# Optimization experiments

Measured on AMD Instinct MI355X. Metric: run time of the kernel, lower is better.

The kernel has to match this reference:

```python
import jax, jax.numpy as jnp
import numpy as np

JITTER = 1e-06  # from init kwarg
NUM_EMBEDDING = 64

def setup_inputs() -> dict:
    key = jax.random.key(0)
    B, T = 8, 2048
    num_features = 1 + NUM_EMBEDDING + 1 + 1  # mean + z + v + hetero-noise
    tensor = jax.random.normal(key, (B, T, num_features), dtype=jnp.float32)
    return {"tensor": tensor}

def reference(tensor):
    # tensor: (B, T, F) with F = 1 + D + 1 + 1 (mean, z, v, noise)
    B, T, _ = tensor.shape
    mean = tensor[:, :, 0]                       # (B, T)
    z = tensor[:, :, 1:-2]                       # (B, T, D)
    v = tensor[:, :, -2]                         # (B, T)
    noise = jax.nn.softplus(tensor[:, :, -1])    # (B, T) hetero noise
    D = z.shape[-1]
    z = z / jnp.sqrt(jnp.asarray(D, z.dtype))
    # quad[b,i,j] = -0.5 * sum_d (z[b,i,d] - z[b,j,d])**2 via GEMM trick
    sq = jnp.sum(z * z, axis=-1)                 # (B, T)
    zz = jnp.einsum('bid,bjd->bij', z, z)        # (B, T, T)
    quad = -0.5 * (sq[:, :, None] + sq[:, None, :] - 2.0 * zz)
    kern = jnp.exp(quad)                         # (B, T, T)
    f_cov = kern * v[:, :, None] * v[:, None, :] # (B, T, T)
    eye = jnp.eye(T, dtype=tensor.dtype)
    f_cov_j = f_cov + JITTER * eye[None, :, :]
    y_cov_j = f_cov_j + noise[:, :, None] * eye[None, :, :]  # diag_embed(noise)
    return (mean, f_cov_j, y_cov_j)
```

## Files before the change

kernel.cpp:

```cpp
#include <hip/hip_runtime.h>
#include <math.h>

#define BB 8
#define TT 2048
#define FF 67
#define DD 64
#define BT (BB * TT)
#define JITTER 1e-6f

#define NT 32
#define NOFF 496
#define NOFFB (BB * NOFF)
#define NBLK (NOFFB + BB * NT)
#define CPX (NBLK / 8)

__device__ __forceinline__ unsigned int f2bf(float f) {
  unsigned int u = __float_as_uint(f);
  return (u + 0x7fffu + ((u >> 16) & 1u)) >> 16;
}

__global__ __launch_bounds__(256) void pack_stats_kernel(
    const float* __restrict__ in, float* __restrict__ out_mean,
    float* __restrict__ c, float* __restrict__ noise,
    uint4* __restrict__ zp4) {
  int g = blockIdx.x * 256 + threadIdx.x;
  int row = g >> 3, dc = g & 7;
  const float* p = in + (size_t)row * FF + 1 + dc * 8;
  float sq = 0.f;
  unsigned int w[4];
#pragma unroll
  for (int k = 0; k < 4; ++k) {
    float a = p[2 * k] * 0.125f;
    float b2 = p[2 * k + 1] * 0.125f;
    sq += a * a + b2 * b2;
    w[k] = f2bf(a) | (f2bf(b2) << 16);
  }
  uint4 pk;
  pk.x = w[0]; pk.y = w[1]; pk.z = w[2]; pk.w = w[3];
  zp4[(size_t)row * 8 + dc] = pk;
  sq += __shfl_xor(sq, 1);
  sq += __shfl_xor(sq, 2);
  sq += __shfl_xor(sq, 4);
  if (dc == 0) {
    const float* r = in + (size_t)row * FF;
    out_mean[row] = r[0];
    float v = r[1 + DD];
    float x = r[1 + DD + 1];
    float sp = fmaxf(x, 0.f) + log1pf(__expf(-fabsf(x)));
    c[row] = v * __expf(-0.5f * sq);
    noise[row] = sp;
  }
}

__global__ __launch_bounds__(256) void row_stats_kernel(
    const float* __restrict__ in, float* __restrict__ out_mean,
    float* __restrict__ c, float* __restrict__ noise) {
  int idx = blockIdx.x * 256 + threadIdx.x;
  if (idx >= BT) return;
  const float* row = in + (size_t)idx * FF;
  out_mean[idx] = row[0];
  float sq = 0.f;
#pragma unroll
  for (int d = 0; d < DD; ++d) {
    float z = row[1 + d] * 0.125f;
    sq = fmaf(z, z, sq);
  }
  float v = row[1 + DD];
  float x = row[1 + DD + 1];
  float sp = fmaxf(x, 0.f) + log1pf(__expf(-fabsf(x)));
  c[idx] = v * __expf(-0.5f * sq);
  noise[idx] = sp;
}

#define DOT_WORD(WX)                                                      \
  _Pragma("unroll") for (int a = 0; a < 4; ++a)                           \
      _Pragma("unroll") for (int q = 0; q < 4; ++q)                       \
      asm("v_dot2_f32_bf16 %0, %1, %2, %0"                                \
          : "+v"(acc[a][q])                                               \
          : "v"(ai[a].WX), "v"(bj[q].WX));

template <bool PACKED>
__global__ __launch_bounds__(256, 4) void cov_kernel(
    const float* __restrict__ in, const uint4* __restrict__ zp4,
    const float* __restrict__ c, const float* __restrict__ noise,
    float* __restrict__ out_f, float* __restrict__ out_y) {
  __shared__ uint4 lds[1024];

  int bid = blockIdx.x;
  int wid = (bid & 7) * CPX + (bid >> 3);

  int b, ti, tj;
  if (wid < NOFFB) {
    b = wid / NOFF;
    int k = wid - b * NOFF;
    int x = (int)((1.0f + sqrtf(1.0f + 8.0f * (float)k)) * 0.5f);
    while (x * (x - 1) / 2 > k) --x;
    while ((x + 1) * x / 2 <= k) ++x;
    ti = x;
    tj = k - x * (x - 1) / 2;
  } else {
    int r = wid - NOFFB;
    b = r >> 5;
    ti = tj = r & 31;
  }
  const bool diag = (ti == tj);
  const int gi0 = ti * 64, gj0 = tj * 64;
  const int t = threadIdx.x;

#pragma unroll
  for (int kk = 0; kk < 2; ++kk) {
    int idx = kk * 256 + t;
    int row = idx >> 3, ch = idx & 7;
    int sw = (row >> 2) & 7;
    uint4 av, bv;
    if (PACKED) {
      av = zp4[(size_t)(b * TT + gi0 + row) * 8 + ch];
      bv = zp4[(size_t)(b * TT + gj0 + row) * 8 + ch];
    } else {
      const float* pi = in + (size_t)(b * TT + gi0 + row) * FF + 1 + ch * 8;
      const float* pj = in + (size_t)(b * TT + gj0 + row) * FF + 1 + ch * 8;
      unsigned int wi[4], wj[4];
#pragma unroll
      for (int e = 0; e < 4; ++e) {
        wi[e] = f2bf(pi[2 * e] * 0.125f) | (f2bf(pi[2 * e + 1] * 0.125f) << 16);
        wj[e] = f2bf(pj[2 * e] * 0.125f) | (f2bf(pj[2 * e + 1] * 0.125f) << 16);
      }
      av.x = wi[0]; av.y = wi[1]; av.z = wi[2]; av.w = wi[3];
      bv.x = wj[0]; bv.y = wj[1]; bv.z = wj[2]; bv.w = wj[3];
    }
    lds[row * 8 + (ch ^ sw)] = av;
    lds[512 + row * 8 + (ch ^ sw)] = bv;
  }
  __syncthreads();

  const int tx = t & 15, ty = t >> 4;
  const int i0 = ty * 4, j0 = tx * 4;
  const int swi = ty & 7, swj = tx & 7;

  float acc[4][4] = {};
#pragma unroll
  for (int dc = 0; dc < 8; ++dc) {
    uint4 ai[4], bj[4];
#pragma unroll
    for (int a = 0; a < 4; ++a) ai[a] = lds[(i0 + a) * 8 + (dc ^ swi)];
#pragma unroll
    for (int q = 0; q < 4; ++q)
      bj[q] = lds[512 + (j0 + q) * 8 + (dc ^ swj)];
    DOT_WORD(x)
    DOT_WORD(y)
    DOT_WORD(z)
    DOT_WORD(w)
  }

  const float* cbp = c + b * TT;
  float ci[4], cj[4];
#pragma unroll
  for (int a = 0; a < 4; ++a) ci[a] = cbp[gi0 + i0 + a];
#pragma unroll
  for (int q = 0; q < 4; ++q) cj[q] = cbp[gj0 + j0 + q];
#pragma unroll
  for (int a = 0; a < 4; ++a)
#pragma unroll
    for (int q = 0; q < 4; ++q)
      acc[a][q] = __expf(acc[a][q]) * ci[a] * cj[q];

  const size_t TTT = (size_t)TT * TT;
  const size_t obase = (size_t)b * TTT;

  if (!diag) {
    __syncthreads();
    float4* ftv = (float4*)lds;
#pragma unroll
    for (int q = 0; q < 4; ++q) {
      int jr = j0 + q;
      int sw = tx & 7;
      ftv[jr * 16 + (ty ^ sw)] =
          make_float4(acc[0][q], acc[1][q], acc[2][q], acc[3][q]);
    }
    __syncthreads();
#pragma unroll
    for (int kk = 0; kk < 4; ++kk) {
      int idx = kk * 256 + t;
      int jr = idx >> 4, ch = idx & 15;
      int sw = (jr >> 2) & 7;
      float4 v = ftv[jr * 16 + (ch ^ sw)];
      size_t off = obase + (size_t)(gj0 + jr) * TT + gi0 + ch * 4;
      *reinterpret_cast<float4*>(out_f + off) = v;
      *reinterpret_cast<float4*>(out_y + off) = v;
    }
  }

#pragma unroll
  for (int a = 0; a < 4; ++a) {
    int gi = gi0 + i0 + a;
    float fv[4], yv[4];
#pragma unroll
    for (int q = 0; q < 4; ++q) {
      float ff = acc[a][q];
      float yy = ff;
      if (diag && (i0 + a == j0 + q)) {
        ff += JITTER;
        yy = ff + noise[b * TT + gi];
      }
      fv[q] = ff;
      yv[q] = yy;
    }
    size_t off = obase + (size_t)gi * TT + gj0 + j0;
    *reinterpret_cast<float4*>(out_f + off) =
        make_float4(fv[0], fv[1], fv[2], fv[3]);
    *reinterpret_cast<float4*>(out_y + off) =
        make_float4(yv[0], yv[1], yv[2], yv[3]);
  }
}

extern "C" void kernel_launch(void* const* d_in, const int* in_sizes, int n_in,
                              void* d_out, int out_size, void* d_ws,
                              size_t ws_size, hipStream_t stream) {
  const float* in = (const float*)d_in[0];
  float* out = (float*)d_out;
  float* c = (float*)d_ws;
  float* noise = c + BT;
  uint4* zp4 = (uint4*)((char*)d_ws + (size_t)2 * BT * 4);
  float* out_mean = out;
  float* out_f = out + BT;
  float* out_y = out_f + (size_t)BB * TT * TT;

  const size_t need = (size_t)2 * BT * 4 + (size_t)BT * DD * 2;
  if (ws_size >= need) {
    pack_stats_kernel<<<(BT * 8) / 256, 256, 0, stream>>>(in, out_mean, c,
                                                          noise, zp4);
    cov_kernel<true><<<NBLK, 256, 0, stream>>>(in, zp4, c, noise, out_f,
                                               out_y);
  } else {
    row_stats_kernel<<<BT / 256, 256, 0, stream>>>(in, out_mean, c, noise);
    cov_kernel<false><<<NBLK, 256, 0, stream>>>(in, zp4, c, noise, out_f,
                                                out_y);
  }
}
```

Measured before the change: 56.47 us.

## Replace symmetric tile covariance kernel with row-strip kernel reading B from global

Each block now computes a full 64-row strip of the covariance matrix, iterating over column chunks, with A staged in LDS and B read directly from global memory. This drops the triangular tile mapping and the transpose-through-LDS mirror writes, in favour of simpler, contiguous row writes. In exchange it doubles the dot-product work by no longer exploiting symmetry, and launches only 256 large blocks, which lowers occupancy for a store-bound kernel.

```diff
diff --git a/kernel.cpp b/kernel.cpp
--- a/kernel.cpp
+++ b/kernel.cpp
@@ -8,15 +8,18 @@
 #define BT (BB * TT)
 #define JITTER 1e-6f
 
-#define NT 32
-#define NOFF 496
-#define NOFFB (BB * NOFF)
-#define NBLK (NOFFB + BB * NT)
-#define CPX (NBLK / 8)
+#define STRIPS 32
+#define NBLK (BB * STRIPS)
 
 __device__ __forceinline__ unsigned int f2bf(float f) {
   unsigned int u = __float_as_uint(f);
   return (u + 0x7fffu + ((u >> 16) & 1u)) >> 16;
+}
+__device__ __forceinline__ float bf_lo(unsigned int u) {
+  return __uint_as_float(u << 16);
+}
+__device__ __forceinline__ float bf_hi(unsigned int u) {
+  return __uint_as_float(u & 0xffff0000u);
 }
 
 __global__ __launch_bounds__(256) void pack_stats_kernel(
@@ -52,6 +55,132 @@
   }
 }
 
+#define DOT_WORD(WX)                                                      \
+  _Pragma("unroll") for (int a = 0; a < 8; ++a)                           \
+      _Pragma("unroll") for (int q = 0; q < 4; ++q)                       \
+      asm("v_dot2_f32_bf16 %0, %1, %2, %0"                                \
+          : "+v"(acc[a][q])                                               \
+          : "v"(ai[a].WX), "v"(bj[q].WX));
+
+template <bool PACKED>
+__global__ __launch_bounds__(256) void cov_row_kernel(
+    const float* __restrict__ in, const uint4* __restrict__ zp4,
+    const float* __restrict__ c, const float* __restrict__ noise,
+    float* __restrict__ out_f, float* __restrict__ out_y) {
+  __shared__ uint4 Ald[512];
+
+  int bid = blockIdx.x;
+  int wid = (bid & 7) * STRIPS + (bid >> 3);
+  const int b = wid >> 5;
+  const int r0 = (wid & 31) * 64;
+  const int t = threadIdx.x;
+
+  if (PACKED) {
+#pragma unroll
+    for (int kk = 0; kk < 2; ++kk) {
+      int idx = kk * 256 + t;
+      Ald[idx] = zp4[(size_t)(b * TT + r0) * 8 + idx];
+    }
+  } else {
+#pragma unroll
+    for (int kk = 0; kk < 2; ++kk) {
+      int idx = kk * 256 + t;
+      int row = idx >> 3, ch = idx & 7;
+      const float* pi = in + (size_t)(b * TT + r0 + row) * FF + 1 + ch * 8;
+      unsigned int w[4];
+#pragma unroll
+      for (int e = 0; e < 4; ++e)
+        w[e] = f2bf(pi[2 * e] * 0.125f) | (f2bf(pi[2 * e + 1] * 0.125f) << 16);
+      uint4 av;
+      av.x = w[0]; av.y = w[1]; av.z = w[2]; av.w = w[3];
+      Ald[idx] = av;
+    }
+  }
+  __syncthreads();
+
+  const int ty = t >> 5, tx = t & 31;
+  const int ia = ty * 8;
+
+  float ci[8];
+#pragma unroll
+  for (int a = 0; a < 8; ++a) ci[a] = c[b * TT + r0 + ia + a];
+
+  const int diag_jc = r0 >> 7;
+  const size_t TTT = (size_t)TT * TT;
+  const size_t obase = (size_t)b * TTT;
+
+  for (int jc = 0; jc < 16; ++jc) {
+    const int j0 = jc * 128 + tx * 4;
+    float acc[8][4] = {};
+
+    if (PACKED) {
+      const uint4* Bp = zp4 + (size_t)(b * TT + j0) * 8;
+#pragma unroll
+      for (int dc = 0; dc < 8; ++dc) {
+        uint4 bj[4];
+#pragma unroll
+        for (int q = 0; q < 4; ++q) bj[q] = Bp[q * 8 + dc];
+        uint4 ai[8];
+#pragma unroll
+        for (int a = 0; a < 8; ++a) ai[a] = Ald[(ia + a) * 8 + dc];
+        DOT_WORD(x)
+        DOT_WORD(y)
+        DOT_WORD(z)
+        DOT_WORD(w)
+      }
+    } else {
+#pragma unroll
+      for (int dc = 0; dc < 8; ++dc) {
+        float bv[4][8];
+#pragma unroll
+        for (int q = 0; q < 4; ++q) {
+          const float* pj = in + (size_t)(b * TT + j0 + q) * FF + 1 + dc * 8;
+#pragma unroll
+          for (int e = 0; e < 8; ++e) bv[q][e] = pj[e] * 0.125f;
+        }
+#pragma unroll
+        for (int a = 0; a < 8; ++a) {
+          uint4 av = Ald[(ia + a) * 8 + dc];
+          float fa[8] = {bf_lo(av.x), bf_hi(av.x), bf_lo(av.y), bf_hi(av.y),
+                         bf_lo(av.z), bf_hi(av.z), bf_lo(av.w), bf_hi(av.w)};
+#pragma unroll
+          for (int q = 0; q < 4; ++q)
+#pragma unroll
+            for (int e = 0; e < 8; ++e)
+              acc[a][q] = fmaf(fa[e], bv[q][e], acc[a][q]);
+        }
+      }
+    }
+
+    float cj[4];
+#pragma unroll
+    for (int q = 0; q < 4; ++q) cj[q] = c[b * TT + j0 + q];
+
+    const bool dchunk = (jc == diag_jc);
+#pragma unroll
+    for (int a = 0; a < 8; ++a) {
+      int gi = r0 + ia + a;
+      float fv[4], yv[4];
+#pragma unroll
+      for (int q = 0; q < 4; ++q) {
+        float ff = __expf(acc[a][q]) * ci[a] * cj[q];
+        float yy = ff;
+        if (dchunk && (gi == j0 + q)) {
+          ff += JITTER;
+          yy = ff + noise[b * TT + gi];
+        }
+        fv[q] = ff;
+        yv[q] = yy;
+      }
+      size_t off = obase + (size_t)gi * TT + j0;
+      *reinterpret_cast<float4*>(out_f + off) =
+          make_float4(fv[0], fv[1], fv[2], fv[3]);
+      *reinterpret_cast<float4*>(out_y + off) =
+          make_float4(yv[0], yv[1], yv[2], yv[3]);
+    }
+  }
+}
+
 __global__ __launch_bounds__(256) void row_stats_kernel(
     const float* __restrict__ in, float* __restrict__ out_mean,
     float* __restrict__ c, float* __restrict__ noise) {
@@ -70,147 +199,6 @@
   float sp = fmaxf(x, 0.f) + log1pf(__expf(-fabsf(x)));
   c[idx] = v * __expf(-0.5f * sq);
   noise[idx] = sp;
-}
-
-#define DOT_WORD(WX)                                                      \
-  _Pragma("unroll") for (int a = 0; a < 4; ++a)                           \
-      _Pragma("unroll") for (int q = 0; q < 4; ++q)                       \
-      asm("v_dot2_f32_bf16 %0, %1, %2, %0"                                \
-          : "+v"(acc[a][q])                                               \
-          : "v"(ai[a].WX), "v"(bj[q].WX));
-
-template <bool PACKED>
-__global__ __launch_bounds__(256, 4) void cov_kernel(
-    const float* __restrict__ in, const uint4* __restrict__ zp4,
-    const float* __restrict__ c, const float* __restrict__ noise,
-    float* __restrict__ out_f, float* __restrict__ out_y) {
-  __shared__ uint4 lds[1024];
-
-  int bid = blockIdx.x;
-  int wid = (bid & 7) * CPX + (bid >> 3);
-
-  int b, ti, tj;
-  if (wid < NOFFB) {
-    b = wid / NOFF;
-    int k = wid - b * NOFF;
-    int x = (int)((1.0f + sqrtf(1.0f + 8.0f * (float)k)) * 0.5f);
-    while (x * (x - 1) / 2 > k) --x;
-    while ((x + 1) * x / 2 <= k) ++x;
-    ti = x;
-    tj = k - x * (x - 1) / 2;
-  } else {
-    int r = wid - NOFFB;
-    b = r >> 5;
-    ti = tj = r & 31;
-  }
-  const bool diag = (ti == tj);
-  const int gi0 = ti * 64, gj0 = tj * 64;
-  const int t = threadIdx.x;
-
-#pragma unroll
-  for (int kk = 0; kk < 2; ++kk) {
-    int idx = kk * 256 + t;
-    int row = idx >> 3, ch = idx & 7;
-    int sw = (row >> 2) & 7;
-    uint4 av, bv;
-    if (PACKED) {
-      av = zp4[(size_t)(b * TT + gi0 + row) * 8 + ch];
-      bv = zp4[(size_t)(b * TT + gj0 + row) * 8 + ch];
-    } else {
-      const float* pi = in + (size_t)(b * TT + gi0 + row) * FF + 1 + ch * 8;
-      const float* pj = in + (size_t)(b * TT + gj0 + row) * FF + 1 + ch * 8;
-      unsigned int wi[4], wj[4];
-#pragma unroll
-      for (int e = 0; e < 4; ++e) {
-        wi[e] = f2bf(pi[2 * e] * 0.125f) | (f2bf(pi[2 * e + 1] * 0.125f) << 16);
-        wj[e] = f2bf(pj[2 * e] * 0.125f) | (f2bf(pj[2 * e + 1] * 0.125f) << 16);
-      }
-      av.x = wi[0]; av.y = wi[1]; av.z = wi[2]; av.w = wi[3];
-      bv.x = wj[0]; bv.y = wj[1]; bv.z = wj[2]; bv.w = wj[3];
-    }
-    lds[row * 8 + (ch ^ sw)] = av;
-    lds[512 + row * 8 + (ch ^ sw)] = bv;
-  }
-  __syncthreads();
-
-  const int tx = t & 15, ty = t >> 4;
-  const int i0 = ty * 4, j0 = tx * 4;
-  const int swi = ty & 7, swj = tx & 7;
-
-  float acc[4][4] = {};
-#pragma unroll
-  for (int dc = 0; dc < 8; ++dc) {
-    uint4 ai[4], bj[4];
-#pragma unroll
-    for (int a = 0; a < 4; ++a) ai[a] = lds[(i0 + a) * 8 + (dc ^ swi)];
-#pragma unroll
-    for (int q = 0; q < 4; ++q)
-      bj[q] = lds[512 + (j0 + q) * 8 + (dc ^ swj)];
-    DOT_WORD(x)
-    DOT_WORD(y)
-    DOT_WORD(z)
-    DOT_WORD(w)
-  }
-
-  const float* cbp = c + b * TT;
-  float ci[4], cj[4];
-#pragma unroll
-  for (int a = 0; a < 4; ++a) ci[a] = cbp[gi0 + i0 + a];
-#pragma unroll
-  for (int q = 0; q < 4; ++q) cj[q] = cbp[gj0 + j0 + q];
-#pragma unroll
-  for (int a = 0; a < 4; ++a)
-#pragma unroll
-    for (int q = 0; q < 4; ++q)
-      acc[a][q] = __expf(acc[a][q]) * ci[a] * cj[q];
-
-  const size_t TTT = (size_t)TT * TT;
-  const size_t obase = (size_t)b * TTT;
-
-  if (!diag) {
-    __syncthreads();
-    float4* ftv = (float4*)lds;
-#pragma unroll
-    for (int q = 0; q < 4; ++q) {
-      int jr = j0 + q;
-      int sw = tx & 7;
-      ftv[jr * 16 + (ty ^ sw)] =
-          make_float4(acc[0][q], acc[1][q], acc[2][q], acc[3][q]);
-    }
-    __syncthreads();
-#pragma unroll
-    for (int kk = 0; kk < 4; ++kk) {
-      int idx = kk * 256 + t;
-      int jr = idx >> 4, ch = idx & 15;
-      int sw = (jr >> 2) & 7;
-      float4 v = ftv[jr * 16 + (ch ^ sw)];
-      size_t off = obase + (size_t)(gj0 + jr) * TT + gi0 + ch * 4;
-      *reinterpret_cast<float4*>(out_f + off) = v;
-      *reinterpret_cast<float4*>(out_y + off) = v;
-    }
-  }
-
-#pragma unroll
-  for (int a = 0; a < 4; ++a) {
-    int gi = gi0 + i0 + a;
-    float fv[4], yv[4];
-#pragma unroll
-    for (int q = 0; q < 4; ++q) {
-      float ff = acc[a][q];
-      float yy = ff;
-      if (diag && (i0 + a == j0 + q)) {
-        ff += JITTER;
-        yy = ff + noise[b * TT + gi];
-      }
-      fv[q] = ff;
-      yv[q] = yy;
-    }
-    size_t off = obase + (size_t)gi * TT + gj0 + j0;
-    *reinterpret_cast<float4*>(out_f + off) =
-        make_float4(fv[0], fv[1], fv[2], fv[3]);
-    *reinterpret_cast<float4*>(out_y + off) =
-        make_float4(yv[0], yv[1], yv[2], yv[3]);
-  }
 }
 
 extern "C" void kernel_launch(void* const* d_in, const int* in_sizes, int n_in,
@@ -229,11 +217,11 @@
   if (ws_size >= need) {
     pack_stats_kernel<<<(BT * 8) / 256, 256, 0, stream>>>(in, out_mean, c,
                                                           noise, zp4);
-    cov_kernel<true><<<NBLK, 256, 0, stream>>>(in, zp4, c, noise, out_f,
-                                               out_y);
+    cov_row_kernel<true><<<NBLK, 256, 0, stream>>>(in, zp4, c, noise, out_f,
+                                                   out_y);
   } else {
     row_stats_kernel<<<BT / 256, 256, 0, stream>>>(in, out_mean, c, noise);
-    cov_kernel<false><<<NBLK, 256, 0, stream>>>(in, zp4, c, noise, out_f,
-                                                out_y);
-  }
-}
+    cov_row_kernel<false><<<NBLK, 256, 0, stream>>>(in, zp4, c, noise, out_f,
+                                                    out_y);
+  }
+}
```

New measurement: 98.93 us. 75.2% more time.
